# Optimization experiments

Measured on AMD Instinct MI355X. Metric: run time of the kernel, lower is better.

## Reference

```python
import jax, jax.numpy as jnp
import numpy as np
import math

L = 192
D = 128
H = 12
C = 24
EPS = 1e-5


def _layernorm(x, w, b):
    mu = jnp.mean(x, axis=-1, keepdims=True)
    var = jnp.var(x, axis=-1, keepdims=True)
    return (x - mu) * jax.lax.rsqrt(var + EPS) * w + b


def setup_inputs() -> dict:
    key = jax.random.key(0)
    ks = jax.random.split(key, 8)
    s = 0.02
    return {
        "z_": jax.random.normal(ks[0], (L, L, D), dtype=jnp.float32),
        "ln_w": jnp.ones((D,), jnp.float32),
        "ln_b": jnp.zeros((D,), jnp.float32),
        "Wq": jax.random.normal(ks[1], (D, H * C), jnp.float32) * s,
        "bq": jnp.zeros((H * C,), jnp.float32),
        "Wk": jax.random.normal(ks[2], (D, H * C), jnp.float32) * s,
        "bk": jnp.zeros((H * C,), jnp.float32),
        "Wv": jax.random.normal(ks[3], (D, H * C), jnp.float32) * s,
        "bv": jnp.zeros((H * C,), jnp.float32),
        "Wb": jax.random.normal(ks[4], (D, H), jnp.float32) * s,
        "bb": jnp.zeros((H,), jnp.float32),
        "Wg": jax.random.normal(ks[5], (D, H * C), jnp.float32) * s,
        "bg": jnp.zeros((H * C,), jnp.float32),
        "Wo": jax.random.normal(ks[6], (H * C, D), jnp.float32) * s,
        "bo": jnp.zeros((D,), jnp.float32),
    }


def reference(z_, ln_w, ln_b, Wq, bq, Wk, bk, Wv, bv, Wb, bb, Wg, bg, Wo, bo):
    sq_c = 1.0 / math.sqrt(C)
    z = _layernorm(z_, ln_w, ln_b)                     # [L, L, D]
    q = (z @ Wq + bq).reshape(L, L, H, C)
    k = (z @ Wk + bk).reshape(L, L, H, C)
    v = (z @ Wv + bv).reshape(L, L, H, C)
    bias = z @ Wb + bb                                 # [L, L, H]
    # att[b, l, kk, h] = sum_c q[b, l, h, c] * k[kk, b_==l? no: kk, b, h, c]
    att = jnp.einsum('blhc,kbhc->blkh', q, k) * sq_c
    # torch: b[None].permute(0,2,1,3) -> add bias[kk, l, h] broadcast over b
    att = att + jnp.transpose(bias, (1, 0, 2))[None, :, :, :]
    att = jax.nn.softmax(att, axis=2)
    o = jnp.einsum('blkh,klhc->blhc', att, v)          # [L, L, H, C]
    g = jax.nn.sigmoid((z @ Wg + bg).reshape(L, L, H, C))
    o = (g * o).reshape(L, L, H * C)
    return o @ Wo + bo
```

## Files before the change

### kernel.cpp

```cpp
#include <hip/hip_runtime.h>
#include <hip/hip_bf16.h>
#include <math.h>

typedef __hip_bfloat16 bf16;
typedef unsigned short u16;
typedef unsigned int u32;
typedef __attribute__((ext_vector_type(8))) short bf16x8;
typedef __attribute__((ext_vector_type(4))) float f32x4;

#define LL 36864

__device__ __forceinline__ float wave_sum(float v) {
#pragma unroll
  for (int m = 32; m; m >>= 1) v += __shfl_xor(v, m, 64);
  return v;
}

__device__ __forceinline__ float bf2f(u16 u) {
  union { float f; u32 u; } c; c.u = ((u32)u) << 16; return c.f;
}
__device__ __forceinline__ u16 f2bf(float f) {
  union { float f; u32 u; } c; c.f = f;
  u32 r = c.u + 0x7fffu + ((c.u >> 16) & 1u);
  return (u16)(r >> 16);
}

__global__ __launch_bounds__(256) void k_cvt(const float* __restrict__ Wq,
                                             const float* __restrict__ Wk,
                                             const float* __restrict__ Wv,
                                             const float* __restrict__ Wg,
                                             bf16* __restrict__ Wcat) {
  int u = blockIdx.x * 256 + threadIdx.x;
  if (u >= 18432) return;
  int jg = u >> 4, k0 = (u & 15) * 8;
  int sec = jg / 288, j = jg % 288;
  const float* W = sec == 0 ? Wq : sec == 1 ? Wk : sec == 2 ? Wv : Wg;
  u16 pk[8];
#pragma unroll
  for (int i = 0; i < 8; ++i) pk[i] = f2bf(W[(size_t)(k0 + i) * 288 + j]);
  *reinterpret_cast<uint4*>(&Wcat[(size_t)jg * 128 + k0]) = *reinterpret_cast<uint4*>(pk);
}

__global__ __launch_bounds__(256) void k_cvt2(const float* __restrict__ Wo,
                                              bf16* __restrict__ Wot) {
  int u = blockIdx.x * 256 + threadIdx.x;
  if (u >= 4608) return;
  int n = u / 36, k0 = (u % 36) * 8;
  u16 pk[8];
#pragma unroll
  for (int i = 0; i < 8; ++i) pk[i] = f2bf(Wo[(size_t)(k0 + i) * 128 + n]);
  *reinterpret_cast<uint4*>(&Wot[(size_t)n * 288 + k0]) = *reinterpret_cast<uint4*>(pk);
}

__global__ __launch_bounds__(256) void k_ln(const float* __restrict__ zin,
                                            const float* __restrict__ w_,
                                            const float* __restrict__ b_,
                                            const float* __restrict__ Wb,
                                            const float* __restrict__ bbv,
                                            bf16* __restrict__ zb,
                                            float* __restrict__ biasb) {
  int t = threadIdx.x;
  int wv = t >> 6, lane = t & 63;
  size_t m = (size_t)blockIdx.x * 4 + wv;
  const float2 v = *reinterpret_cast<const float2*>(&zin[m * 128 + lane * 2]);
  float s = wave_sum(v.x + v.y);
  float ss = wave_sum(v.x * v.x + v.y * v.y);
  float mean = s * (1.0f / 128.0f);
  float var = ss * (1.0f / 128.0f) - mean * mean;
  float rs = rsqrtf(var + 1e-5f);
  float o0 = (v.x - mean) * rs * w_[lane * 2] + b_[lane * 2];
  float o1 = (v.y - mean) * rs * w_[lane * 2 + 1] + b_[lane * 2 + 1];
  u32 pk = (u32)f2bf(o0) | ((u32)f2bf(o1) << 16);
  *reinterpret_cast<u32*>(&zb[m * 128 + lane * 2]) = pk;
  float accb[12];
#pragma unroll
  for (int h = 0; h < 12; ++h)
    accb[h] = o0 * Wb[(lane * 2) * 12 + h] + o1 * Wb[(lane * 2 + 1) * 12 + h];
#pragma unroll
  for (int h = 0; h < 12; ++h) accb[h] = wave_sum(accb[h]);
  if (lane == 0) {
    int kk = (int)m / 192, l = (int)m % 192;
#pragma unroll
    for (int h = 0; h < 12; ++h)
      biasb[(size_t)h * LL + (size_t)l * 192 + kk] = accb[h] + bbv[h];
  }
}

__global__ __launch_bounds__(256) void k_proj(const bf16* __restrict__ zb,
    const bf16* __restrict__ Wcat,
    const float* __restrict__ bq, const float* __restrict__ bk,
    const float* __restrict__ bv, const float* __restrict__ bg,
    bf16* __restrict__ q2, bf16* __restrict__ k2,
    bf16* __restrict__ vb, bf16* __restrict__ gbuf) {
  __shared__ __align__(16) u16 Sb[192 * 104];
  int t = threadIdx.x;
  int w = t >> 6, lane = t & 63;
  int c15 = lane & 15, g = lane >> 4;
  int wm = w & 1, wn = w >> 1;
  int bx = blockIdx.x, y = blockIdx.y;
  int sec = y / 3, h0 = (y % 3) * 4;
  int m0 = bx * 192;
  int jbase = y * 96;
  f32x4 acc[6][3];
#pragma unroll
  for (int mt = 0; mt < 6; ++mt)
#pragma unroll
    for (int nt = 0; nt < 3; ++nt) acc[mt][nt] = (f32x4){0.f, 0.f, 0.f, 0.f};
#pragma unroll
  for (int kt = 0; kt < 4; ++kt) {
    bf16x8 a[6], b[3];
#pragma unroll
    for (int mt = 0; mt < 6; ++mt)
      a[mt] = *reinterpret_cast<const bf16x8*>(
          &zb[(size_t)(m0 + wm * 96 + mt * 16 + c15) * 128 + kt * 32 + g * 8]);
#pragma unroll
    for (int nt = 0; nt < 3; ++nt)
      b[nt] = *reinterpret_cast<const bf16x8*>(
          &Wcat[(size_t)(jbase + wn * 48 + nt * 16 + c15) * 128 + kt * 32 + g * 8]);
#pragma unroll
    for (int mt = 0; mt < 6; ++mt)
#pragma unroll
      for (int nt = 0; nt < 3; ++nt)
        acc[mt][nt] = __builtin_amdgcn_mfma_f32_16x16x32_bf16(a[mt], b[nt], acc[mt][nt], 0, 0, 0);
  }
  const float* barr = sec == 0 ? bq : sec == 1 ? bk : sec == 2 ? bv : bg;
#pragma unroll
  for (int nt = 0; nt < 3; ++nt) {
    int col = wn * 48 + nt * 16 + c15;
    float bval = barr[(y % 3) * 96 + col];
#pragma unroll
    for (int mt = 0; mt < 6; ++mt) {
      int rbase = wm * 96 + mt * 16 + 4 * g;
#pragma unroll
      for (int i = 0; i < 4; ++i)
        Sb[(rbase + i) * 104 + col] = f2bf(acc[mt][nt][i] + bval);
    }
  }
  __syncthreads();
  if (sec == 0) {
    bf16* dst0 = q2 + ((size_t)bx * 12 + h0) * 4608;
    for (int u = t; u < 2304; u += 256) {
      int hl = u / 576, off = (u % 576) * 8;
      int ml = off / 24, c0 = off % 24;
      uint4 val = *reinterpret_cast<const uint4*>(&Sb[ml * 104 + hl * 24 + c0]);
      *reinterpret_cast<uint4*>(&dst0[(size_t)hl * 4608 + off]) = val;
    }
  } else if (sec == 3) {
    for (int u = t; u < 2304; u += 256) {
      int ml = u / 12, col = (u % 12) * 8;
      uint4 val = *reinterpret_cast<const uint4*>(&Sb[ml * 104 + col]);
      *reinterpret_cast<uint4*>(&gbuf[(size_t)(m0 + ml) * 288 + h0 * 24 + col]) = val;
    }
  } else {
    bf16* dst = (sec == 1) ? k2 : vb;
    for (int u = t; u < 2304; u += 256) {
      int hl = u / 576, off = (u % 576) * 8;
      int ml = off / 24, c0 = off % 24;
      uint4 val = *reinterpret_cast<const uint4*>(&Sb[ml * 104 + hl * 24 + c0]);
      *reinterpret_cast<uint4*>(
          &dst[(((size_t)ml * 12 + h0 + hl) * 192 + bx) * 24 + c0]) = val;
    }
  }
}

__global__ __launch_bounds__(256) void k_attpv(const bf16* __restrict__ q2,
    const bf16* __restrict__ k2, const float* __restrict__ biasb,
    const bf16* __restrict__ vbuf, const bf16* __restrict__ gbuf,
    bf16* __restrict__ Patt, const bf16* __restrict__ Ppv,
    bf16* __restrict__ ogb, int la0, int lp0, int NT, int NL) {
  __shared__ __align__(16) char ldsraw[25600];
  int t = threadIdx.x;
  int w = t >> 6, lane = t & 63;
  int c15 = lane & 15, g = lane >> 4;
  const float sq_c = 0.20412414523193154f;
  bool is_att = (la0 >= 0) && (gridDim.z == 1 || blockIdx.z == 0);
  if (is_att) {
    int x = blockIdx.x, h = blockIdx.y;
    int bq = x * 4 + w;
    u16* Sb = reinterpret_cast<u16*>(ldsraw) + (size_t)w * 3200;
    const bf16* ks = &k2[((size_t)bq * 12 + h) * 4608];
    const float* bsrc = &biasb[(size_t)h * LL];
    for (int lt = 0; lt < NT; ++lt) {
      int l0 = la0 + lt * 16;
      const bf16* qs = &q2[(((size_t)bq * 12 + h) * 192 + l0) * 24];
      bf16x8 afr = {0, 0, 0, 0, 0, 0, 0, 0};
      if (g < 3) afr = *reinterpret_cast<const bf16x8*>(&qs[c15 * 24 + g * 8]);
      f32x4 acc[12];
#pragma unroll
      for (int ct = 0; ct < 12; ++ct) {
        bf16x8 bfr = {0, 0, 0, 0, 0, 0, 0, 0};
        if (g < 3) bfr = *reinterpret_cast<const bf16x8*>(&ks[(ct * 16 + c15) * 24 + g * 8]);
        acc[ct] = __builtin_amdgcn_mfma_f32_16x16x32_bf16(afr, bfr, (f32x4){0.f, 0.f, 0.f, 0.f}, 0, 0, 0);
      }
#pragma unroll
      for (int i = 0; i < 4; ++i) {
        int l = l0 + 4 * g + i;
#pragma unroll
        for (int ct = 0; ct < 12; ++ct)
          acc[ct][i] = acc[ct][i] * sq_c + bsrc[(size_t)l * 192 + ct * 16 + c15];
      }
      float inv[4];
#pragma unroll
      for (int i = 0; i < 4; ++i) {
        float mx = -1e30f;
#pragma unroll
        for (int ct = 0; ct < 12; ++ct) mx = fmaxf(mx, acc[ct][i]);
#pragma unroll
        for (int msk = 1; msk < 16; msk <<= 1) mx = fmaxf(mx, __shfl_xor(mx, msk, 64));
        float sm = 0.f;
#pragma unroll
        for (int ct = 0; ct < 12; ++ct) {
          float e = __expf(acc[ct][i] - mx);
          acc[ct][i] = e;
          sm += e;
        }
#pragma unroll
        for (int msk = 1; msk < 16; msk <<= 1) sm += __shfl_xor(sm, msk, 64);
        inv[i] = 1.0f / sm;
      }
#pragma unroll
      for (int i = 0; i < 4; ++i)
#pragma unroll
        for (int ct = 0; ct < 12; ++ct)
          Sb[(4 * g + i) * 200 + ct * 16 + c15] = f2bf(acc[ct][i] * inv[i]);
      int lrel = l0 - la0;
      for (int u = lane; u < 384; u += 64) {
        int lloc = u / 24, oct = u % 24;
        uint4 val = *reinterpret_cast<const uint4*>(&Sb[lloc * 200 + oct * 8]);
        *reinterpret_cast<uint4*>(
            &Patt[(((size_t)(lrel + lloc) * 12 + h) * 192 + bq) * 192 + oct * 8]) = val;
      }
    }
  } else {
    if (lp0 < 0) return;
    int x = blockIdx.x, h = blockIdx.y;
    if (x >= NL) return;
    u16* Vt = reinterpret_cast<u16*>(ldsraw);
    float* Ob = reinterpret_cast<float*>(ldsraw + 12800) + (size_t)w * 416;
    int l = lp0 + x;
    int lrel = x;
    const bf16* vs = &vbuf[((size_t)l * 12 + h) * 4608];
    for (int u = t; u < 576; u += 256) {
      int kk = u / 3, c0 = (u % 3) * 8;
      uint4 val = *reinterpret_cast<const uint4*>(&vs[kk * 24 + c0]);
      const u16* pv = reinterpret_cast<const u16*>(&val);
#pragma unroll
      for (int i = 0; i < 8; ++i) Vt[(c0 + i) * 200 + kk] = pv[i];
    }
    __syncthreads();
    bf16x8 bfr[6][2];
#pragma unroll
    for (int kt = 0; kt < 6; ++kt)
#pragma unroll
      for (int nt = 0; nt < 2; ++nt)
        bfr[kt][nt] = *reinterpret_cast<const bf16x8*>(
            &Vt[(nt * 16 + c15) * 200 + kt * 32 + g * 8]);
    const bf16* Ps = &Ppv[((size_t)lrel * 12 + h) * 36864];
#pragma unroll
    for (int mi = 0; mi < 3; ++mi) {
      int mt = w * 3 + mi;
      f32x4 acc0 = (f32x4){0.f, 0.f, 0.f, 0.f};
      f32x4 acc1 = (f32x4){0.f, 0.f, 0.f, 0.f};
#pragma unroll
      for (int kt = 0; kt < 6; ++kt) {
        bf16x8 a = *reinterpret_cast<const bf16x8*>(
            &Ps[(size_t)(mt * 16 + c15) * 192 + kt * 32 + g * 8]);
        acc0 = __builtin_amdgcn_mfma_f32_16x16x32_bf16(a, bfr[kt][0], acc0, 0, 0, 0);
        acc1 = __builtin_amdgcn_mfma_f32_16x16x32_bf16(a, bfr[kt][1], acc1, 0, 0, 0);
      }
#pragma unroll
      for (int i = 0; i < 4; ++i) {
        Ob[(4 * g + i) * 26 + c15] = acc0[i];
        if (c15 < 8) Ob[(4 * g + i) * 26 + 16 + c15] = acc1[i];
      }
      if (lane < 48) {
        int r = lane / 3, c0 = (lane % 3) * 8;
        int b = mt * 16 + r;
        size_t m = (size_t)b * 192 + l;
        uint4 gv4 = *reinterpret_cast<const uint4*>(&gbuf[m * 288 + h * 24 + c0]);
        const u16* gp = reinterpret_cast<const u16*>(&gv4);
        u16 opk[8];
#pragma unroll
        for (int i = 0; i < 8; ++i) {
          float av = Ob[r * 26 + c0 + i];
          float sg = 1.0f / (1.0f + __expf(-bf2f(gp[i])));
          opk[i] = f2bf(av * sg);
        }
        *reinterpret_cast<uint4*>(&ogb[m * 288 + h * 24 + c0]) = *reinterpret_cast<uint4*>(opk);
      }
    }
  }
}

__global__ __launch_bounds__(256) void k_out(const bf16* __restrict__ ogb,
                                             const bf16* __restrict__ Wot,
                                             const float* __restrict__ bo,
                                             float* __restrict__ out) {
  int t = threadIdx.x;
  int w = t >> 6, lane = t & 63;
  int c15 = lane & 15, g = lane >> 4;
  int m0 = blockIdx.x * 64;
  int mrow = m0 + w * 16 + c15;
  f32x4 acc[8];
#pragma unroll
  for (int nt = 0; nt < 8; ++nt) acc[nt] = (f32x4){0.f, 0.f, 0.f, 0.f};
#pragma unroll
  for (int kt = 0; kt < 9; ++kt) {
    bf16x8 a = *reinterpret_cast<const bf16x8*>(&ogb[(size_t)mrow * 288 + kt * 32 + g * 8]);
    bf16x8 b[8];
#pragma unroll
    for (int nt = 0; nt < 8; ++nt)
      b[nt] = *reinterpret_cast<const bf16x8*>(&Wot[(size_t)(nt * 16 + c15) * 288 + kt * 32 + g * 8]);
#pragma unroll
    for (int nt = 0; nt < 8; ++nt)
      acc[nt] = __builtin_amdgcn_mfma_f32_16x16x32_bf16(a, b[nt], acc[nt], 0, 0, 0);
  }
#pragma unroll
  for (int nt = 0; nt < 8; ++nt) {
    int n = nt * 16 + c15;
    float bval = bo[n];
#pragma unroll
    for (int i = 0; i < 4; ++i) {
      int m = m0 + w * 16 + 4 * g + i;
      out[(size_t)m * 128 + n] = acc[nt][i] + bval;
    }
  }
}

extern "C" void kernel_launch(void* const* d_in, const int* in_sizes, int n_in,
                              void* d_out, int out_size, void* d_ws, size_t ws_size,
                              hipStream_t stream) {
  const float* z_in = (const float*)d_in[0];
  const float* ln_w = (const float*)d_in[1];
  const float* ln_b = (const float*)d_in[2];
  const float* Wq   = (const float*)d_in[3];
  const float* bq   = (const float*)d_in[4];
  const float* Wk   = (const float*)d_in[5];
  const float* bk   = (const float*)d_in[6];
  const float* Wv   = (const float*)d_in[7];
  const float* bv   = (const float*)d_in[8];
  const float* Wb   = (const float*)d_in[9];
  const float* bb   = (const float*)d_in[10];
  const float* Wg   = (const float*)d_in[11];
  const float* bg   = (const float*)d_in[12];
  const float* Wo   = (const float*)d_in[13];
  const float* bo   = (const float*)d_in[14];
  float* out = (float*)d_out;

  char* ws = (char*)d_ws;
  bf16* q2    = (bf16*)(ws + 0);
  bf16* k2    = (bf16*)(ws + 21233664);
  bf16* vb    = (bf16*)(ws + 42467328);
  bf16* gbuf  = (bf16*)(ws + 63700992);
  bf16* ogb   = (bf16*)(ws + 84934656);
  bf16* zb    = (bf16*)(ws + 84934656);
  bf16* Wcat  = (bf16*)(ws + 94371840);
  float* biasb = (float*)(ws + 106168320);
  char* Pbase = ws + 107937792;
  bf16* Wot   = (bf16*)(ws + 107937792);

  k_cvt<<<dim3(72), dim3(256), 0, stream>>>(Wq, Wk, Wv, Wg, Wcat);
  k_ln<<<dim3(9216), dim3(256), 0, stream>>>(z_in, ln_w, ln_b, Wb, bb, zb, biasb);
  k_proj<<<dim3(192, 12), dim3(256), 0, stream>>>(zb, Wcat, bq, bk, bv, bg,
                                                  q2, k2, vb, gbuf);
  const size_t PB = 107937792ull;
  int CL;
  if      (ws_size >= PB + 169869312ull) CL = 192;
  else if (ws_size >= PB + 84934656ull)  CL = 48;
  else if (ws_size >= PB + 56623104ull)  CL = 32;
  else if (ws_size >= PB + 28311552ull)  CL = 16;
  else                                   CL = -16;
  if (CL == 192) {
    bf16* P = (bf16*)Pbase;
    k_attpv<<<dim3(48, 12, 1), dim3(256), 0, stream>>>(
        q2, k2, biasb, vb, gbuf, P, P, ogb, 0, -1, 12, 192);
    k_attpv<<<dim3(192, 12, 1), dim3(256), 0, stream>>>(
        q2, k2, biasb, vb, gbuf, P, P, ogb, -1, 0, 12, 192);
  } else if (CL > 0) {
    int nch = 192 / CL;
    size_t csz = (size_t)CL * 884736ull;
    bf16* P0 = (bf16*)Pbase;
    bf16* P1 = (bf16*)(Pbase + csz);
    int NT = CL / 16;
    for (int n = 0; n <= nch; ++n) {
      bf16* Pa = (n & 1) ? P1 : P0;
      bf16* Pp = ((n - 1) & 1) ? P1 : P0;
      int la = (n < nch) ? n * CL : -1;
      int lp = (n >= 1) ? (n - 1) * CL : -1;
      if (la >= 0 && lp >= 0)
        k_attpv<<<dim3(48 > CL ? 48 : CL, 12, 2), dim3(256), 0, stream>>>(
            q2, k2, biasb, vb, gbuf, Pa, Pp, ogb, la, lp, NT, CL);
      else if (la >= 0)
        k_attpv<<<dim3(48, 12, 1), dim3(256), 0, stream>>>(
            q2, k2, biasb, vb, gbuf, Pa, Pp, ogb, la, -1, NT, CL);
      else
        k_attpv<<<dim3(CL, 12, 1), dim3(256), 0, stream>>>(
            q2, k2, biasb, vb, gbuf, Pa, Pp, ogb, -1, lp, NT, CL);
    }
  } else {
    bf16* P0 = (bf16*)Pbase;
    for (int n = 0; n < 12; ++n) {
      k_attpv<<<dim3(48, 12, 1), dim3(256), 0, stream>>>(
          q2, k2, biasb, vb, gbuf, P0, P0, ogb, n * 16, -1, 1, 16);
      k_attpv<<<dim3(16, 12, 1), dim3(256), 0, stream>>>(
          q2, k2, biasb, vb, gbuf, P0, P0, ogb, -1, n * 16, 1, 16);
    }
  }
  k_cvt2<<<dim3(18), dim3(256), 0, stream>>>(Wo, Wot);
  k_out<<<dim3(576), dim3(256), 0, stream>>>(ogb, Wot, bo, out);
}
```

Baseline: 254.4 us.

## Swap MFMA operands to transpose accumulator layout for vectorized epilogues

Swaps the A and B operands of the MFMA calls in the projection, attention-score and PV kernels, so each lane holds four consecutive columns of one row instead of four rows of one column. The epilogues are rewritten to match: bias is read as float4, results are packed into uint2 bf16 stores, the softmax max and sum need only two cross-lane shuffles instead of four per row, and the PV gating reads the gate and writes directly from registers without the LDS staging buffer. The aim is fewer scalar LDS and global accesses, fewer shuffles and no extra LDS round trip in the gating step. Correctness depends on the transposed indexing being consistent everywhere it is used.

Result: slower. 271.9 us (+6.9%).

```diff
diff --git a/kernel.cpp b/kernel.cpp
--- a/kernel.cpp
+++ b/kernel.cpp
@@ -23,6 +23,9 @@
   union { float f; u32 u; } c; c.f = f;
   u32 r = c.u + 0x7fffu + ((c.u >> 16) & 1u);
   return (u16)(r >> 16);
+}
+__device__ __forceinline__ float sigf(float x) {
+  return 1.0f / (1.0f + __expf(-x));
 }
 
 __global__ __launch_bounds__(256) void k_cvt(const float* __restrict__ Wq,
@@ -121,19 +124,26 @@
     for (int mt = 0; mt < 6; ++mt)
 #pragma unroll
       for (int nt = 0; nt < 3; ++nt)
-        acc[mt][nt] = __builtin_amdgcn_mfma_f32_16x16x32_bf16(a[mt], b[nt], acc[mt][nt], 0, 0, 0);
+        acc[mt][nt] = __builtin_amdgcn_mfma_f32_16x16x32_bf16(b[nt], a[mt], acc[mt][nt], 0, 0, 0);
   }
   const float* barr = sec == 0 ? bq : sec == 1 ? bk : sec == 2 ? bv : bg;
-#pragma unroll
-  for (int nt = 0; nt < 3; ++nt) {
-    int col = wn * 48 + nt * 16 + c15;
-    float bval = barr[(y % 3) * 96 + col];
-#pragma unroll
-    for (int mt = 0; mt < 6; ++mt) {
-      int rbase = wm * 96 + mt * 16 + 4 * g;
-#pragma unroll
-      for (int i = 0; i < 4; ++i)
-        Sb[(rbase + i) * 104 + col] = f2bf(acc[mt][nt][i] + bval);
+  float4 bias4[3];
+#pragma unroll
+  for (int nt = 0; nt < 3; ++nt)
+    bias4[nt] = *reinterpret_cast<const float4*>(
+        &barr[(y % 3) * 96 + wn * 48 + nt * 16 + 4 * g]);
+#pragma unroll
+  for (int mt = 0; mt < 6; ++mt) {
+    int row = wm * 96 + mt * 16 + c15;
+#pragma unroll
+    for (int nt = 0; nt < 3; ++nt) {
+      int col = wn * 48 + nt * 16 + 4 * g;
+      uint2 pk;
+      pk.x = (u32)f2bf(acc[mt][nt][0] + bias4[nt].x) |
+             ((u32)f2bf(acc[mt][nt][1] + bias4[nt].y) << 16);
+      pk.y = (u32)f2bf(acc[mt][nt][2] + bias4[nt].z) |
+             ((u32)f2bf(acc[mt][nt][3] + bias4[nt].w) << 16);
+      *reinterpret_cast<uint2*>(&Sb[row * 104 + col]) = pk;
     }
   }
   __syncthreads();
@@ -190,39 +200,43 @@
       for (int ct = 0; ct < 12; ++ct) {
         bf16x8 bfr = {0, 0, 0, 0, 0, 0, 0, 0};
         if (g < 3) bfr = *reinterpret_cast<const bf16x8*>(&ks[(ct * 16 + c15) * 24 + g * 8]);
-        acc[ct] = __builtin_amdgcn_mfma_f32_16x16x32_bf16(afr, bfr, (f32x4){0.f, 0.f, 0.f, 0.f}, 0, 0, 0);
-      }
-#pragma unroll
-      for (int i = 0; i < 4; ++i) {
-        int l = l0 + 4 * g + i;
-#pragma unroll
-        for (int ct = 0; ct < 12; ++ct)
-          acc[ct][i] = acc[ct][i] * sq_c + bsrc[(size_t)l * 192 + ct * 16 + c15];
-      }
-      float inv[4];
-#pragma unroll
-      for (int i = 0; i < 4; ++i) {
-        float mx = -1e30f;
-#pragma unroll
-        for (int ct = 0; ct < 12; ++ct) mx = fmaxf(mx, acc[ct][i]);
-#pragma unroll
-        for (int msk = 1; msk < 16; msk <<= 1) mx = fmaxf(mx, __shfl_xor(mx, msk, 64));
-        float sm = 0.f;
-#pragma unroll
-        for (int ct = 0; ct < 12; ++ct) {
+        acc[ct] = __builtin_amdgcn_mfma_f32_16x16x32_bf16(bfr, afr, (f32x4){0.f, 0.f, 0.f, 0.f}, 0, 0, 0);
+      }
+      const float* brow = &bsrc[(size_t)(l0 + c15) * 192];
+#pragma unroll
+      for (int ct = 0; ct < 12; ++ct) {
+        float4 b4 = *reinterpret_cast<const float4*>(&brow[ct * 16 + 4 * g]);
+        acc[ct][0] = acc[ct][0] * sq_c + b4.x;
+        acc[ct][1] = acc[ct][1] * sq_c + b4.y;
+        acc[ct][2] = acc[ct][2] * sq_c + b4.z;
+        acc[ct][3] = acc[ct][3] * sq_c + b4.w;
+      }
+      float mx = -1e30f;
+#pragma unroll
+      for (int ct = 0; ct < 12; ++ct)
+#pragma unroll
+        for (int i = 0; i < 4; ++i) mx = fmaxf(mx, acc[ct][i]);
+      mx = fmaxf(mx, __shfl_xor(mx, 16, 64));
+      mx = fmaxf(mx, __shfl_xor(mx, 32, 64));
+      float sm = 0.f;
+#pragma unroll
+      for (int ct = 0; ct < 12; ++ct)
+#pragma unroll
+        for (int i = 0; i < 4; ++i) {
           float e = __expf(acc[ct][i] - mx);
           acc[ct][i] = e;
           sm += e;
         }
-#pragma unroll
-        for (int msk = 1; msk < 16; msk <<= 1) sm += __shfl_xor(sm, msk, 64);
-        inv[i] = 1.0f / sm;
-      }
-#pragma unroll
-      for (int i = 0; i < 4; ++i)
-#pragma unroll
-        for (int ct = 0; ct < 12; ++ct)
-          Sb[(4 * g + i) * 200 + ct * 16 + c15] = f2bf(acc[ct][i] * inv[i]);
+      sm += __shfl_xor(sm, 16, 64);
+      sm += __shfl_xor(sm, 32, 64);
+      float inv = 1.0f / sm;
+#pragma unroll
+      for (int ct = 0; ct < 12; ++ct) {
+        uint2 pk;
+        pk.x = (u32)f2bf(acc[ct][0] * inv) | ((u32)f2bf(acc[ct][1] * inv) << 16);
+        pk.y = (u32)f2bf(acc[ct][2] * inv) | ((u32)f2bf(acc[ct][3] * inv) << 16);
+        *reinterpret_cast<uint2*>(&Sb[c15 * 200 + ct * 16 + 4 * g]) = pk;
+      }
       int lrel = l0 - la0;
       for (int u = lane; u < 384; u += 64) {
         int lloc = u / 24, oct = u % 24;
@@ -236,7 +250,6 @@
     int x = blockIdx.x, h = blockIdx.y;
     if (x >= NL) return;
     u16* Vt = reinterpret_cast<u16*>(ldsraw);
-    float* Ob = reinterpret_cast<float*>(ldsraw + 12800) + (size_t)w * 416;
     int l = lp0 + x;
     int lrel = x;
     const bf16* vs = &vbuf[((size_t)l * 12 + h) * 4608];
@@ -265,28 +278,30 @@
       for (int kt = 0; kt < 6; ++kt) {
         bf16x8 a = *reinterpret_cast<const bf16x8*>(
             &Ps[(size_t)(mt * 16 + c15) * 192 + kt * 32 + g * 8]);
-        acc0 = __builtin_amdgcn_mfma_f32_16x16x32_bf16(a, bfr[kt][0], acc0, 0, 0, 0);
-        acc1 = __builtin_amdgcn_mfma_f32_16x16x32_bf16(a, bfr[kt][1], acc1, 0, 0, 0);
-      }
-#pragma unroll
-      for (int i = 0; i < 4; ++i) {
-        Ob[(4 * g + i) * 26 + c15] = acc0[i];
-        if (c15 < 8) Ob[(4 * g + i) * 26 + 16 + c15] = acc1[i];
-      }
-      if (lane < 48) {
-        int r = lane / 3, c0 = (lane % 3) * 8;
-        int b = mt * 16 + r;
-        size_t m = (size_t)b * 192 + l;
-        uint4 gv4 = *reinterpret_cast<const uint4*>(&gbuf[m * 288 + h * 24 + c0]);
-        const u16* gp = reinterpret_cast<const u16*>(&gv4);
-        u16 opk[8];
-#pragma unroll
-        for (int i = 0; i < 8; ++i) {
-          float av = Ob[r * 26 + c0 + i];
-          float sg = 1.0f / (1.0f + __expf(-bf2f(gp[i])));
-          opk[i] = f2bf(av * sg);
-        }
-        *reinterpret_cast<uint4*>(&ogb[m * 288 + h * 24 + c0]) = *reinterpret_cast<uint4*>(opk);
+        acc0 = __builtin_amdgcn_mfma_f32_16x16x32_bf16(bfr[kt][0], a, acc0, 0, 0, 0);
+        acc1 = __builtin_amdgcn_mfma_f32_16x16x32_bf16(bfr[kt][1], a, acc1, 0, 0, 0);
+      }
+      int b = mt * 16 + c15;
+      size_t m = (size_t)b * 192 + l;
+      {
+        int c0 = 4 * g;
+        uint2 g4 = *reinterpret_cast<const uint2*>(&gbuf[m * 288 + h * 24 + c0]);
+        uint2 pk;
+        pk.x = (u32)f2bf(acc0[0] * sigf(bf2f((u16)(g4.x & 0xffff)))) |
+               ((u32)f2bf(acc0[1] * sigf(bf2f((u16)(g4.x >> 16)))) << 16);
+        pk.y = (u32)f2bf(acc0[2] * sigf(bf2f((u16)(g4.y & 0xffff)))) |
+               ((u32)f2bf(acc0[3] * sigf(bf2f((u16)(g4.y >> 16)))) << 16);
+        *reinterpret_cast<uint2*>(&ogb[m * 288 + h * 24 + c0]) = pk;
+      }
+      if (g < 2) {
+        int c0 = 16 + 4 * g;
+        uint2 g4 = *reinterpret_cast<const uint2*>(&gbuf[m * 288 + h * 24 + c0]);
+        uint2 pk;
+        pk.x = (u32)f2bf(acc1[0] * sigf(bf2f((u16)(g4.x & 0xffff)))) |
+               ((u32)f2bf(acc1[1] * sigf(bf2f((u16)(g4.x >> 16)))) << 16);
+        pk.y = (u32)f2bf(acc1[2] * sigf(bf2f((u16)(g4.y & 0xffff)))) |
+               ((u32)f2bf(acc1[3] * sigf(bf2f((u16)(g4.y >> 16)))) << 16);
+        *reinterpret_cast<uint2*>(&ogb[m * 288 + h * 24 + c0]) = pk;
       }
     }
   }
```

## Retile projection GEMM to full-section columns and stage bias rows in LDS

Applied to the files above, without the earlier changes.

The projection kernel now uses 96-row by 288-column tiles, one full section (q/k/v/g) per block. It stages the z tile in LDS, swaps the MFMA operands so each lane writes packed bf16x4 runs, and writes all 12 heads per block with a reworked scatter. The point is to reuse the z tile across all heads of a section and make the output stores contiguous. Separately, the attention kernel cooperatively loads the 16x192 bias slice into LDS for each l-tile instead of each wave issuing strided global loads. This adds two block barriers per tile and raises LDS usage, which may lower occupancy.

Measured after the change: 273.1 us. +7.4%, slower.

```diff
diff --git a/kernel.cpp b/kernel.cpp
--- a/kernel.cpp
+++ b/kernel.cpp
@@ -92,73 +92,87 @@
     const float* __restrict__ bv, const float* __restrict__ bg,
     bf16* __restrict__ q2, bf16* __restrict__ k2,
     bf16* __restrict__ vb, bf16* __restrict__ gbuf) {
-  __shared__ __align__(16) u16 Sb[192 * 104];
+  __shared__ __align__(16) u16 SB[96 * 292];
   int t = threadIdx.x;
   int w = t >> 6, lane = t & 63;
   int c15 = lane & 15, g = lane >> 4;
   int wm = w & 1, wn = w >> 1;
   int bx = blockIdx.x, y = blockIdx.y;
-  int sec = y / 3, h0 = (y % 3) * 4;
-  int m0 = bx * 192;
-  int jbase = y * 96;
-  f32x4 acc[6][3];
-#pragma unroll
-  for (int mt = 0; mt < 6; ++mt)
-#pragma unroll
-    for (int nt = 0; nt < 3; ++nt) acc[mt][nt] = (f32x4){0.f, 0.f, 0.f, 0.f};
+  int m0 = bx * 96;
+  int jb = y * 288;
+  for (int f = t; f < 1536; f += 256) {
+    int r = f >> 4, c8 = f & 15;
+    uint4 v = *reinterpret_cast<const uint4*>(&zb[(size_t)(m0 + r) * 128 + c8 * 8]);
+    *reinterpret_cast<uint4*>(&SB[r * 136 + c8 * 8]) = v;
+  }
+  __syncthreads();
+  int rb = wm * 48;
+  f32x4 acc[3][9];
+#pragma unroll
+  for (int mt = 0; mt < 3; ++mt)
+#pragma unroll
+    for (int nt = 0; nt < 9; ++nt) acc[mt][nt] = (f32x4){0.f, 0.f, 0.f, 0.f};
 #pragma unroll
   for (int kt = 0; kt < 4; ++kt) {
-    bf16x8 a[6], b[3];
-#pragma unroll
-    for (int mt = 0; mt < 6; ++mt)
+    bf16x8 a[3], b[9];
+#pragma unroll
+    for (int mt = 0; mt < 3; ++mt)
       a[mt] = *reinterpret_cast<const bf16x8*>(
-          &zb[(size_t)(m0 + wm * 96 + mt * 16 + c15) * 128 + kt * 32 + g * 8]);
-#pragma unroll
-    for (int nt = 0; nt < 3; ++nt)
+          &SB[(rb + mt * 16 + c15) * 136 + kt * 32 + g * 8]);
+#pragma unroll
+    for (int nt = 0; nt < 9; ++nt)
       b[nt] = *reinterpret_cast<const bf16x8*>(
-          &Wcat[(size_t)(jbase + wn * 48 + nt * 16 + c15) * 128 + kt * 32 + g * 8]);
-#pragma unroll
-    for (int mt = 0; mt < 6; ++mt)
-#pragma unroll
-      for (int nt = 0; nt < 3; ++nt)
-        acc[mt][nt] = __builtin_amdgcn_mfma_f32_16x16x32_bf16(a[mt], b[nt], acc[mt][nt], 0, 0, 0);
-  }
-  const float* barr = sec == 0 ? bq : sec == 1 ? bk : sec == 2 ? bv : bg;
-#pragma unroll
-  for (int nt = 0; nt < 3; ++nt) {
-    int col = wn * 48 + nt * 16 + c15;
-    float bval = barr[(y % 3) * 96 + col];
-#pragma unroll
-    for (int mt = 0; mt < 6; ++mt) {
-      int rbase = wm * 96 + mt * 16 + 4 * g;
-#pragma unroll
-      for (int i = 0; i < 4; ++i)
-        Sb[(rbase + i) * 104 + col] = f2bf(acc[mt][nt][i] + bval);
-    }
-  }
+          &Wcat[(size_t)(jb + wn * 144 + nt * 16 + c15) * 128 + kt * 32 + g * 8]);
+#pragma unroll
+    for (int mt = 0; mt < 3; ++mt)
+#pragma unroll
+      for (int nt = 0; nt < 9; ++nt)
+        acc[mt][nt] = __builtin_amdgcn_mfma_f32_16x16x32_bf16(b[nt], a[mt], acc[mt][nt], 0, 0, 0);
+  }
+  const float* barr = y == 0 ? bq : y == 1 ? bk : y == 2 ? bv : bg;
+  float4 bias4[9];
+#pragma unroll
+  for (int nt = 0; nt < 9; ++nt)
+    bias4[nt] = *reinterpret_cast<const float4*>(&barr[wn * 144 + nt * 16 + 4 * g]);
   __syncthreads();
-  if (sec == 0) {
-    bf16* dst0 = q2 + ((size_t)bx * 12 + h0) * 4608;
-    for (int u = t; u < 2304; u += 256) {
-      int hl = u / 576, off = (u % 576) * 8;
-      int ml = off / 24, c0 = off % 24;
-      uint4 val = *reinterpret_cast<const uint4*>(&Sb[ml * 104 + hl * 24 + c0]);
-      *reinterpret_cast<uint4*>(&dst0[(size_t)hl * 4608 + off]) = val;
-    }
-  } else if (sec == 3) {
-    for (int u = t; u < 2304; u += 256) {
-      int ml = u / 12, col = (u % 12) * 8;
-      uint4 val = *reinterpret_cast<const uint4*>(&Sb[ml * 104 + col]);
-      *reinterpret_cast<uint4*>(&gbuf[(size_t)(m0 + ml) * 288 + h0 * 24 + col]) = val;
+#pragma unroll
+  for (int mt = 0; mt < 3; ++mt) {
+    int row = rb + mt * 16 + c15;
+#pragma unroll
+    for (int nt = 0; nt < 9; ++nt) {
+      int col = wn * 144 + nt * 16 + 4 * g;
+      uint2 pk;
+      pk.x = (u32)f2bf(acc[mt][nt][0] + bias4[nt].x) |
+             ((u32)f2bf(acc[mt][nt][1] + bias4[nt].y) << 16);
+      pk.y = (u32)f2bf(acc[mt][nt][2] + bias4[nt].z) |
+             ((u32)f2bf(acc[mt][nt][3] + bias4[nt].w) << 16);
+      *reinterpret_cast<uint2*>(&SB[row * 292 + col]) = pk;
+    }
+  }
+  __syncthreads();
+  int bhalf = bx >> 1, rlo = (bx & 1) * 96;
+  if (y == 3) {
+    for (int f = t; f < 3456; f += 256) {
+      int row = f / 36, seg = f % 36;
+      uint4 val = *reinterpret_cast<const uint4*>(&SB[row * 292 + seg * 8]);
+      *reinterpret_cast<uint4*>(&gbuf[(size_t)(m0 + row) * 288 + seg * 8]) = val;
     }
   } else {
-    bf16* dst = (sec == 1) ? k2 : vb;
-    for (int u = t; u < 2304; u += 256) {
-      int hl = u / 576, off = (u % 576) * 8;
-      int ml = off / 24, c0 = off % 24;
-      uint4 val = *reinterpret_cast<const uint4*>(&Sb[ml * 104 + hl * 24 + c0]);
-      *reinterpret_cast<uint4*>(
-          &dst[(((size_t)ml * 12 + h0 + hl) * 192 + bx) * 24 + c0]) = val;
+    for (int f = t; f < 3456; f += 256) {
+      int row = f / 36, seg = f % 36;
+      int h = seg / 3, c0 = (seg % 3) * 8;
+      uint4 val = *reinterpret_cast<const uint4*>(&SB[row * 292 + h * 24 + c0]);
+      size_t addr;
+      if (y == 0) {
+        addr = (((size_t)bhalf * 12 + h) * 192 + (rlo + row)) * 24 + c0;
+        *reinterpret_cast<uint4*>(&q2[addr]) = val;
+      } else if (y == 1) {
+        addr = (((size_t)(rlo + row) * 12 + h) * 192 + bhalf) * 24 + c0;
+        *reinterpret_cast<uint4*>(&k2[addr]) = val;
+      } else {
+        addr = (((size_t)(rlo + row) * 12 + h) * 192 + bhalf) * 24 + c0;
+        *reinterpret_cast<uint4*>(&vb[addr]) = val;
+      }
     }
   }
 }
@@ -168,7 +182,7 @@
     const bf16* __restrict__ vbuf, const bf16* __restrict__ gbuf,
     bf16* __restrict__ Patt, const bf16* __restrict__ Ppv,
     bf16* __restrict__ ogb, int la0, int lp0, int NT, int NL) {
-  __shared__ __align__(16) char ldsraw[25600];
+  __shared__ __align__(16) char ldsraw[38144];
   int t = threadIdx.x;
   int w = t >> 6, lane = t & 63;
   int c15 = lane & 15, g = lane >> 4;
@@ -177,11 +191,19 @@
   if (is_att) {
     int x = blockIdx.x, h = blockIdx.y;
     int bq = x * 4 + w;
-    u16* Sb = reinterpret_cast<u16*>(ldsraw) + (size_t)w * 3200;
+    float* Lb = reinterpret_cast<float*>(ldsraw);
+    u16* Sb = reinterpret_cast<u16*>(ldsraw + 12544) + (size_t)w * 3200;
     const bf16* ks = &k2[((size_t)bq * 12 + h) * 4608];
     const float* bsrc = &biasb[(size_t)h * LL];
     for (int lt = 0; lt < NT; ++lt) {
       int l0 = la0 + lt * 16;
+      __syncthreads();
+      for (int u = t; u < 768; u += 256) {
+        int r = u / 48, c4 = (u % 48) * 4;
+        *reinterpret_cast<float4*>(&Lb[r * 196 + c4]) =
+            *reinterpret_cast<const float4*>(&bsrc[(size_t)(l0 + r) * 192 + c4]);
+      }
+      __syncthreads();
       const bf16* qs = &q2[(((size_t)bq * 12 + h) * 192 + l0) * 24];
       bf16x8 afr = {0, 0, 0, 0, 0, 0, 0, 0};
       if (g < 3) afr = *reinterpret_cast<const bf16x8*>(&qs[c15 * 24 + g * 8]);
@@ -193,12 +215,10 @@
         acc[ct] = __builtin_amdgcn_mfma_f32_16x16x32_bf16(afr, bfr, (f32x4){0.f, 0.f, 0.f, 0.f}, 0, 0, 0);
       }
 #pragma unroll
-      for (int i = 0; i < 4; ++i) {
-        int l = l0 + 4 * g + i;
+      for (int i = 0; i < 4; ++i)
 #pragma unroll
         for (int ct = 0; ct < 12; ++ct)
-          acc[ct][i] = acc[ct][i] * sq_c + bsrc[(size_t)l * 192 + ct * 16 + c15];
-      }
+          acc[ct][i] = acc[ct][i] * sq_c + Lb[(4 * g + i) * 196 + ct * 16 + c15];
       float inv[4];
 #pragma unroll
       for (int i = 0; i < 4; ++i) {
@@ -361,8 +381,8 @@
 
   k_cvt<<<dim3(72), dim3(256), 0, stream>>>(Wq, Wk, Wv, Wg, Wcat);
   k_ln<<<dim3(9216), dim3(256), 0, stream>>>(z_in, ln_w, ln_b, Wb, bb, zb, biasb);
-  k_proj<<<dim3(192, 12), dim3(256), 0, stream>>>(zb, Wcat, bq, bk, bv, bg,
-                                                  q2, k2, vb, gbuf);
+  k_proj<<<dim3(384, 4), dim3(256), 0, stream>>>(zb, Wcat, bq, bk, bv, bg,
+                                                 q2, k2, vb, gbuf);
   const size_t PB = 107937792ull;
   int CL;
   if      (ws_size >= PB + 169869312ull) CL = 192;
```

## Permute bias layout, fold log2e into softmax, gate PV outputs directly from registers

Applied to the files above, without the earlier changes.

The bias buffer is stored with a permuted key index and pre-scaled by log2(e). Each attention lane can then load its 12 bias values with three float4 reads and use exp2 instead of exp. The PV kernel swaps MFMA operand order so accumulators map straight to output rows, which removes the LDS staging buffer before the sigmoid gating and store. A CL=64 chunking tier and an early-exit guard for attention blocks are also added.

Measured after the change: 299.3 us. +17.7%, slower.

```diff
diff --git a/kernel.cpp b/kernel.cpp
--- a/kernel.cpp
+++ b/kernel.cpp
@@ -9,6 +9,7 @@
 typedef __attribute__((ext_vector_type(4))) float f32x4;
 
 #define LL 36864
+#define LOG2E 1.4426950408889634f
 
 __device__ __forceinline__ float wave_sum(float v) {
 #pragma unroll
@@ -80,9 +81,10 @@
   for (int h = 0; h < 12; ++h) accb[h] = wave_sum(accb[h]);
   if (lane == 0) {
     int kk = (int)m / 192, l = (int)m % 192;
+    int p = (kk & 15) * 12 + (kk >> 4);
 #pragma unroll
     for (int h = 0; h < 12; ++h)
-      biasb[(size_t)h * LL + (size_t)l * 192 + kk] = accb[h] + bbv[h];
+      biasb[(size_t)h * LL + (size_t)l * 192 + p] = (accb[h] + bbv[h]) * LOG2E;
   }
 }
 
@@ -172,10 +174,11 @@
   int t = threadIdx.x;
   int w = t >> 6, lane = t & 63;
   int c15 = lane & 15, g = lane >> 4;
-  const float sq_c = 0.20412414523193154f;
+  const float sq_c2 = 0.20412414523193154f * LOG2E;
   bool is_att = (la0 >= 0) && (gridDim.z == 1 || blockIdx.z == 0);
   if (is_att) {
     int x = blockIdx.x, h = blockIdx.y;
+    if (x >= 48) return;
     int bq = x * 4 + w;
     u16* Sb = reinterpret_cast<u16*>(ldsraw) + (size_t)w * 3200;
     const bf16* ks = &k2[((size_t)bq * 12 + h) * 4608];
@@ -194,10 +197,15 @@
       }
 #pragma unroll
       for (int i = 0; i < 4; ++i) {
-        int l = l0 + 4 * g + i;
+        const float* bT = &bsrc[(size_t)(l0 + 4 * g + i) * 192 + c15 * 12];
+        float4 b0 = *reinterpret_cast<const float4*>(&bT[0]);
+        float4 b1 = *reinterpret_cast<const float4*>(&bT[4]);
+        float4 b2 = *reinterpret_cast<const float4*>(&bT[8]);
+        float bb12[12] = {b0.x, b0.y, b0.z, b0.w, b1.x, b1.y, b1.z, b1.w,
+                          b2.x, b2.y, b2.z, b2.w};
 #pragma unroll
         for (int ct = 0; ct < 12; ++ct)
-          acc[ct][i] = acc[ct][i] * sq_c + bsrc[(size_t)l * 192 + ct * 16 + c15];
+          acc[ct][i] = acc[ct][i] * sq_c2 + bb12[ct];
       }
       float inv[4];
 #pragma unroll
@@ -210,7 +218,7 @@
         float sm = 0.f;
 #pragma unroll
         for (int ct = 0; ct < 12; ++ct) {
-          float e = __expf(acc[ct][i] - mx);
+          float e = exp2f(acc[ct][i] - mx);
           acc[ct][i] = e;
           sm += e;
         }
@@ -236,7 +244,6 @@
     int x = blockIdx.x, h = blockIdx.y;
     if (x >= NL) return;
     u16* Vt = reinterpret_cast<u16*>(ldsraw);
-    float* Ob = reinterpret_cast<float*>(ldsraw + 12800) + (size_t)w * 416;
     int l = lp0 + x;
     int lrel = x;
     const bf16* vs = &vbuf[((size_t)l * 12 + h) * 4608];
@@ -265,28 +272,30 @@
       for (int kt = 0; kt < 6; ++kt) {
         bf16x8 a = *reinterpret_cast<const bf16x8*>(
             &Ps[(size_t)(mt * 16 + c15) * 192 + kt * 32 + g * 8]);
-        acc0 = __builtin_amdgcn_mfma_f32_16x16x32_bf16(a, bfr[kt][0], acc0, 0, 0, 0);
-        acc1 = __builtin_amdgcn_mfma_f32_16x16x32_bf16(a, bfr[kt][1], acc1, 0, 0, 0);
-      }
-#pragma unroll
-      for (int i = 0; i < 4; ++i) {
-        Ob[(4 * g + i) * 26 + c15] = acc0[i];
-        if (c15 < 8) Ob[(4 * g + i) * 26 + 16 + c15] = acc1[i];
-      }
-      if (lane < 48) {
-        int r = lane / 3, c0 = (lane % 3) * 8;
-        int b = mt * 16 + r;
-        size_t m = (size_t)b * 192 + l;
-        uint4 gv4 = *reinterpret_cast<const uint4*>(&gbuf[m * 288 + h * 24 + c0]);
-        const u16* gp = reinterpret_cast<const u16*>(&gv4);
-        u16 opk[8];
-#pragma unroll
-        for (int i = 0; i < 8; ++i) {
-          float av = Ob[r * 26 + c0 + i];
-          float sg = 1.0f / (1.0f + __expf(-bf2f(gp[i])));
-          opk[i] = f2bf(av * sg);
-        }
-        *reinterpret_cast<uint4*>(&ogb[m * 288 + h * 24 + c0]) = *reinterpret_cast<uint4*>(opk);
+        acc0 = __builtin_amdgcn_mfma_f32_16x16x32_bf16(bfr[kt][0], a, acc0, 0, 0, 0);
+        acc1 = __builtin_amdgcn_mfma_f32_16x16x32_bf16(bfr[kt][1], a, acc1, 0, 0, 0);
+      }
+      int b = mt * 16 + c15;
+      size_t m = (size_t)b * 192 + l;
+      {
+        int c0 = 4 * g;
+        uint2 g4 = *reinterpret_cast<const uint2*>(&gbuf[m * 288 + h * 24 + c0]);
+        uint2 pk;
+        pk.x = (u32)f2bf(acc0[0] / (1.0f + __expf(-bf2f((u16)(g4.x & 0xffff))))) |
+               ((u32)f2bf(acc0[1] / (1.0f + __expf(-bf2f((u16)(g4.x >> 16))))) << 16);
+        pk.y = (u32)f2bf(acc0[2] / (1.0f + __expf(-bf2f((u16)(g4.y & 0xffff))))) |
+               ((u32)f2bf(acc0[3] / (1.0f + __expf(-bf2f((u16)(g4.y >> 16))))) << 16);
+        *reinterpret_cast<uint2*>(&ogb[m * 288 + h * 24 + c0]) = pk;
+      }
+      if (g < 2) {
+        int c0 = 16 + 4 * g;
+        uint2 g4 = *reinterpret_cast<const uint2*>(&gbuf[m * 288 + h * 24 + c0]);
+        uint2 pk;
+        pk.x = (u32)f2bf(acc1[0] / (1.0f + __expf(-bf2f((u16)(g4.x & 0xffff))))) |
+               ((u32)f2bf(acc1[1] / (1.0f + __expf(-bf2f((u16)(g4.x >> 16))))) << 16);
+        pk.y = (u32)f2bf(acc1[2] / (1.0f + __expf(-bf2f((u16)(g4.y & 0xffff))))) |
+               ((u32)f2bf(acc1[3] / (1.0f + __expf(-bf2f((u16)(g4.y >> 16))))) << 16);
+        *reinterpret_cast<uint2*>(&ogb[m * 288 + h * 24 + c0]) = pk;
       }
     }
   }
@@ -366,6 +375,7 @@
   const size_t PB = 107937792ull;
   int CL;
   if      (ws_size >= PB + 169869312ull) CL = 192;
+  else if (ws_size >= PB + 113246208ull) CL = 64;
   else if (ws_size >= PB + 84934656ull)  CL = 48;
   else if (ws_size >= PB + 56623104ull)  CL = 32;
   else if (ws_size >= PB + 28311552ull)  CL = 16;
```
